# Performance work log

Hardware: AMD Instinct MI355X
Metric: run time of the kernel (lower is better)

Reference implementation:

```python
import jax, jax.numpy as jnp
import numpy as np

B, T, V, E, H = 256, 512, 30000, 256, 32


def _run_dir(x, mask, Wih, Whh, bih, bhh, reverse):
    # x: [B,T,D], mask: [B,T] bool. PyTorch GRU gate order: r, z, n.
    gi = jnp.einsum('btd,gd->btg', x, Wih) + bih  # precompute input gates [B,T,3H]
    h0 = jnp.zeros((x.shape[0], Whh.shape[1]), x.dtype)

    def step(h, inp):
        gi_t, m_t = inp
        gh = h @ Whh.T + bhh
        ir, iz, inn = jnp.split(gi_t, 3, axis=-1)
        hr, hz, hn = jnp.split(gh, 3, axis=-1)
        r = jax.nn.sigmoid(ir + hr)
        z = jax.nn.sigmoid(iz + hz)
        n = jnp.tanh(inn + r * hn)
        h_new = (1.0 - z) * n + z * h
        # packed-sequence semantics: freeze state at padded steps
        h = jnp.where(m_t[:, None], h_new, h)
        return h, h

    hT, ys = jax.lax.scan(step, h0, (jnp.swapaxes(gi, 0, 1), mask.T), reverse=reverse)
    return jnp.swapaxes(ys, 0, 1), hT  # outputs [B,T,H], final hidden [B,H]


def _bigru_layer(x, mask, pf, pb):
    of, hf = _run_dir(x, mask, *pf, reverse=False)
    ob, hb = _run_dir(x, mask, *pb, reverse=True)
    return jnp.concatenate([of, ob], axis=-1), hf, hb


def setup_inputs() -> dict:
    key = jax.random.key(0)
    ks = jax.random.split(key, 24)
    lengths = jax.random.randint(ks[0], (B,), 1, T + 1)
    mask = (jnp.arange(T)[None, :] < lengths[:, None]).astype(jnp.int32)
    ids = jax.random.randint(ks[1], (B, T), 1, V)
    ids = jnp.where(mask > 0, ids, 0)  # pad_id = 0 at padded positions
    embed = (jax.random.normal(ks[2], (V, E), jnp.float32) * 0.1).at[0].set(0.0)

    def gru_params(k, din):
        k1, k2, k3, k4 = jax.random.split(k, 4)
        s = 1.0 / np.sqrt(H)
        return (jax.random.uniform(k1, (3 * H, din), jnp.float32, -s, s),
                jax.random.uniform(k2, (3 * H, H), jnp.float32, -s, s),
                jax.random.uniform(k3, (3 * H,), jnp.float32, -s, s),
                jax.random.uniform(k4, (3 * H,), jnp.float32, -s, s))

    inp = {"input_ids": ids, "attention_mask": mask, "embed": embed}
    i = 3
    for layer, din in (("l0", E), ("l1", 2 * H)):
        for d in ("f", "b"):
            Wih, Whh, bih, bhh = gru_params(ks[i], din); i += 1
            inp[f"Wih_{layer}{d}"] = Wih
            inp[f"Whh_{layer}{d}"] = Whh
            inp[f"bih_{layer}{d}"] = bih
            inp[f"bhh_{layer}{d}"] = bhh
    s = 1.0 / np.sqrt(2 * H)
    inp["Wout"] = jax.random.uniform(ks[i], (6, 2 * H), jnp.float32, -s, s)
    inp["bout"] = jax.random.uniform(ks[i + 1], (6,), jnp.float32, -s, s)
    return inp


def reference(input_ids, attention_mask, embed,
              Wih_l0f, Whh_l0f, bih_l0f, bhh_l0f,
              Wih_l0b, Whh_l0b, bih_l0b, bhh_l0b,
              Wih_l1f, Whh_l1f, bih_l1f, bhh_l1f,
              Wih_l1b, Whh_l1b, bih_l1b, bhh_l1b,
              Wout, bout):
    mask = attention_mask > 0
    x = embed[input_ids]  # [B,T,E]
    x1, _, _ = _bigru_layer(x, mask,
                            (Wih_l0f, Whh_l0f, bih_l0f, bhh_l0f),
                            (Wih_l0b, Whh_l0b, bih_l0b, bhh_l0b))
    # no dropout: eval-mode forward
    _, hf, hb = _bigru_layer(x1, mask,
                             (Wih_l1f, Whh_l1f, bih_l1f, bhh_l1f),
                             (Wih_l1b, Whh_l1b, bih_l1b, bhh_l1b))
    top = jnp.concatenate([hf, hb], axis=-1)  # h_n[-2:] -> [B, 2H]
    return top @ Wout.T + bout  # [B, 6]
```

## Files before the change

### kernel.cpp

```cpp
#include <hip/hip_runtime.h>
#include <hip/hip_bf16.h>

#define B_ 256
#define T_ 512
#define V_ 30000
#define E_ 256
#define H_ 32

__device__ __forceinline__ float sigmoidf_fast(float x) {
    return 1.0f / (1.0f + __expf(-x));
}
__device__ __forceinline__ float tanhf_fast(float x) {
    return 1.0f - 2.0f / (1.0f + __expf(2.0f * x));
}
__device__ __forceinline__ float rl(float v, int lane) {
    return __int_as_float(__builtin_amdgcn_readlane(__float_as_int(v), lane));
}

#define GEMM_MT 64
#define GEMM_KC 32
#define GEMM_PA 68
#define GEMM_PB 196

__global__ __launch_bounds__(256) void gemm_gates(
    const float* __restrict__ A, int M, int K,
    const float* __restrict__ Wf, const float* __restrict__ Wb,
    const float* __restrict__ bihf, const float* __restrict__ bhhf,
    const float* __restrict__ bihb, const float* __restrict__ bhhb,
    float* __restrict__ Out)
{
    __shared__ float As[GEMM_KC][GEMM_PA];
    __shared__ float Bs[GEMM_KC][GEMM_PB];

    const int tid = threadIdx.x;
    const int mbase = blockIdx.x * GEMM_MT;
    const int mg = tid >> 5, ng = tid & 31;
    const int m_off = mg * 8, n_off = ng * 6;

    float acc[8][6];
    #pragma unroll
    for (int r = 0; r < 8; ++r)
        #pragma unroll
        for (int c = 0; c < 6; ++c) acc[r][c] = 0.f;

    for (int kc = 0; kc < K; kc += GEMM_KC) {
        #pragma unroll
        for (int i = 0; i < 2; ++i) {
            int fi = tid + 256 * i;
            int row = fi >> 3, cf = fi & 7;
            int m = mbase + row;
            float4 v = make_float4(0.f, 0.f, 0.f, 0.f);
            if (m < M) v = *(const float4*)&A[(size_t)m * K + kc + cf * 4];
            As[cf * 4 + 0][row] = v.x; As[cf * 4 + 1][row] = v.y;
            As[cf * 4 + 2][row] = v.z; As[cf * 4 + 3][row] = v.w;
        }
        #pragma unroll
        for (int i = 0; i < 6; ++i) {
            int fi = tid + 256 * i;
            int g = fi >> 3, cf = fi & 7;
            const float* Wsel = (g < 96) ? (Wf + (size_t)g * K)
                                         : (Wb + (size_t)(g - 96) * K);
            float4 v = *(const float4*)&Wsel[kc + cf * 4];
            Bs[cf * 4 + 0][g] = v.x; Bs[cf * 4 + 1][g] = v.y;
            Bs[cf * 4 + 2][g] = v.z; Bs[cf * 4 + 3][g] = v.w;
        }
        __syncthreads();
        #pragma unroll
        for (int k = 0; k < GEMM_KC; ++k) {
            float a[8], bb[6];
            *(float4*)&a[0] = *(const float4*)&As[k][m_off];
            *(float4*)&a[4] = *(const float4*)&As[k][m_off + 4];
            *(float2*)&bb[0] = *(const float2*)&Bs[k][n_off];
            *(float2*)&bb[2] = *(const float2*)&Bs[k][n_off + 2];
            *(float2*)&bb[4] = *(const float2*)&Bs[k][n_off + 4];
            #pragma unroll
            for (int r = 0; r < 8; ++r)
                #pragma unroll
                for (int c = 0; c < 6; ++c)
                    acc[r][c] = fmaf(a[r], bb[c], acc[r][c]);
        }
        __syncthreads();
    }

    float bias[6];
    #pragma unroll
    for (int c = 0; c < 6; ++c) {
        int g = n_off + c;
        int g96 = (g < 96) ? g : g - 96;
        const float* bih = (g < 96) ? bihf : bihb;
        const float* bhh = (g < 96) ? bhhf : bhhb;
        bias[c] = bih[g96] + ((g96 < 64) ? bhh[g96] : 0.f);
    }
    #pragma unroll
    for (int r = 0; r < 8; ++r) {
        int m = mbase + m_off + r;
        if (m < M) {
            float* op = &Out[(size_t)m * 192 + n_off];
            #pragma unroll
            for (int c = 0; c < 6; ++c) op[c] = acc[r][c] + bias[c];
        }
    }
}

template <int USE_IDS>
__global__ __launch_bounds__(64, 1) void gru_scan(
    const float* __restrict__ gi,
    const int* __restrict__ ids,
    const int* __restrict__ mask,
    const float* __restrict__ Whh_f, const float* __restrict__ Whh_b,
    const float* __restrict__ bhh_f, const float* __restrict__ bhh_b,
    float* __restrict__ out_seq,
    float* __restrict__ out_fin)
{
    const int l = threadIdx.x;
    const int j = l & 31;
    const bool lower = l < 32;
    const int dir = blockIdx.x & 1;
    const int b = blockIdx.x >> 1;
    const int bT = b * T_;

    const float* Whh = dir ? Whh_b : Whh_f;
    const float* bhh = dir ? bhh_b : bhh_f;

    const int rowA = lower ? j : (32 + j);
    float wA[32], wB[32];
    #pragma unroll
    for (int q = 0; q < 8; ++q) {
        float4 a = *(const float4*)&Whh[rowA * 32 + q * 4];
        wA[q * 4 + 0] = a.x; wA[q * 4 + 1] = a.y;
        wA[q * 4 + 2] = a.z; wA[q * 4 + 3] = a.w;
        float4 bq = *(const float4*)&Whh[(64 + j) * 32 + q * 4];
        wB[q * 4 + 0] = bq.x; wB[q * 4 + 1] = bq.y;
        wB[q * 4 + 2] = bq.z; wB[q * 4 + 3] = bq.w;
    }
    const float bn = bhh[64 + j];
    const int offA = dir * 96 + l;
    const int offB = dir * 96 + 64 + j;

    auto wbase = [&](int c) { return dir ? (bT + 508 - 4 * c) : (bT + 4 * c); };

    int4 ids0 = make_int4(0, 0, 0, 0);
    if (USE_IDS) ids0 = *(const int4*)&ids[wbase(0)];
    int4 mask_use = *(const int4*)&mask[wbase(0)];
    int4 mask_mid = *(const int4*)&mask[wbase(1)];
    int4 mask_in  = make_int4(0, 0, 0, 0);
    int4 ids_pf = make_int4(0, 0, 0, 0), ids_mid = ids_pf, ids_in = ids_pf;
    if (USE_IDS) {
        ids_pf  = *(const int4*)&ids[wbase(1)];
        ids_mid = *(const int4*)&ids[wbase(2)];
    }

    float gA[2][4], gB[2][4];
    #pragma unroll
    for (int u = 0; u < 4; ++u) {
        int row;
        if (USE_IDS) {
            const int* ip = (const int*)&ids0;
            row = dir ? ip[3 - u] : ip[u];
        } else {
            row = bT + (dir ? (511 - u) : u);
        }
        const float* gp = gi + (size_t)row * 192;
        gA[0][u] = gp[offA];
        gB[0][u] = gp[offB];
    }

    float h = 0.f;

    for (int c2 = 0; c2 < 64; ++c2) {
        #pragma unroll
        for (int p = 0; p < 2; ++p) {
            const int c = 2 * c2 + p;
            if (USE_IDS) {
                const int ci = (c + 3 < 128) ? (c + 3) : 127;
                ids_in = *(const int4*)&ids[wbase(ci)];
            }
            {
                const int cm = (c + 2 < 128) ? (c + 2) : 127;
                mask_in = *(const int4*)&mask[wbase(cm)];
            }
            const int cN = (c + 1 < 128) ? (c + 1) : 127;

            #pragma unroll
            for (int u = 0; u < 4; ++u) {
                int rowN;
                if (USE_IDS) {
                    const int* ip = (const int*)&ids_pf;
                    rowN = dir ? ip[3 - u] : ip[u];
                } else {
                    rowN = bT + (dir ? (511 - 4 * cN - u) : (4 * cN + u));
                }
                const float* gpN = gi + (size_t)rowN * 192;
                gA[p ^ 1][u] = gpN[offA];
                gB[p ^ 1][u] = gpN[offB];

                const int* mu = (const int*)&mask_use;
                const int m = dir ? mu[3 - u] : mu[u];

                float aA0 = 0.f, aA1 = 0.f, aA2 = 0.f, aA3 = 0.f;
                float aB0 = 0.f, aB1 = 0.f, aB2 = 0.f, aB3 = 0.f;
                #pragma unroll
                for (int k = 0; k < 32; k += 4) {
                    const float h0 = rl(h, k);
                    const float h1 = rl(h, k + 1);
                    const float h2 = rl(h, k + 2);
                    const float h3 = rl(h, k + 3);
                    aA0 = fmaf(wA[k],     h0, aA0);  aB0 = fmaf(wB[k],     h0, aB0);
                    aA1 = fmaf(wA[k + 1], h1, aA1);  aB1 = fmaf(wB[k + 1], h1, aB1);
                    aA2 = fmaf(wA[k + 2], h2, aA2);  aB2 = fmaf(wB[k + 2], h2, aB2);
                    aA3 = fmaf(wA[k + 3], h3, aA3);  aB3 = fmaf(wB[k + 3], h3, aB3);
                }
                const float dA = (aA0 + aA1) + (aA2 + aA3);
                const float dB = (aB0 + aB1) + (aB2 + aB3);

                const float s  = sigmoidf_fast(gA[p][u] + dA);
                const float hn = bn + dB;
                const float zz = __shfl_xor(s, 32, 64);
                const float n  = tanhf_fast(gB[p][u] + s * hn);
                const float hnew = n + zz * (h - n);
                h = m ? hnew : h;

                if (out_seq != nullptr) {
                    const int t = dir ? (511 - 4 * c - u) : (4 * c + u);
                    if (lower)
                        out_seq[(size_t)(bT + t) * 64 + dir * 32 + j] = h;
                }
            }
            mask_use = mask_mid; mask_mid = mask_in;
            if (USE_IDS) { ids_pf = ids_mid; ids_mid = ids_in; }
        }
    }

    if (out_fin != nullptr && lower)
        out_fin[b * 64 + dir * 32 + j] = h;
}

__global__ void head_kernel(const float* __restrict__ hfin,
                            const float* __restrict__ Wout,
                            const float* __restrict__ bout,
                            float* __restrict__ out)
{
    int idx = blockIdx.x * blockDim.x + threadIdx.x;
    if (idx >= B_ * 6) return;
    int b = idx / 6, o = idx % 6;
    float acc = bout[o];
    const float* hp = hfin + b * 64;
    const float* wp = Wout + o * 64;
    #pragma unroll
    for (int k = 0; k < 64; ++k) acc = fmaf(hp[k], wp[k], acc);
    out[idx] = acc;
}

extern "C" void kernel_launch(void* const* d_in, const int* in_sizes, int n_in,
                              void* d_out, int out_size, void* d_ws, size_t ws_size,
                              hipStream_t stream)
{
    const int*   ids   = (const int*)d_in[0];
    const int*   mask  = (const int*)d_in[1];
    const float* embed = (const float*)d_in[2];
    const float* Wih0f = (const float*)d_in[3];
    const float* Whh0f = (const float*)d_in[4];
    const float* bih0f = (const float*)d_in[5];
    const float* bhh0f = (const float*)d_in[6];
    const float* Wih0b = (const float*)d_in[7];
    const float* Whh0b = (const float*)d_in[8];
    const float* bih0b = (const float*)d_in[9];
    const float* bhh0b = (const float*)d_in[10];
    const float* Wih1f = (const float*)d_in[11];
    const float* Whh1f = (const float*)d_in[12];
    const float* bih1f = (const float*)d_in[13];
    const float* bhh1f = (const float*)d_in[14];
    const float* Wih1b = (const float*)d_in[15];
    const float* Whh1b = (const float*)d_in[16];
    const float* bih1b = (const float*)d_in[17];
    const float* bhh1b = (const float*)d_in[18];
    const float* Wout  = (const float*)d_in[19];
    const float* bout  = (const float*)d_in[20];

    float* ws   = (float*)d_ws;
    float* gbuf = ws;
    float* x1   = ws + (size_t)B_ * T_ * 192;
    float* hfin = x1 + (size_t)B_ * T_ * 64;

    gemm_gates<<<(V_ + GEMM_MT - 1) / GEMM_MT, 256, 0, stream>>>(
        embed, V_, E_, Wih0f, Wih0b, bih0f, bhh0f, bih0b, bhh0b, gbuf);

    gru_scan<1><<<2 * B_, 64, 0, stream>>>(
        gbuf, ids, mask, Whh0f, Whh0b, bhh0f, bhh0b, x1, nullptr);

    gemm_gates<<<(B_ * T_) / GEMM_MT, 256, 0, stream>>>(
        x1, B_ * T_, 64, Wih1f, Wih1b, bih1f, bhh1f, bih1b, bhh1b, gbuf);

    gru_scan<0><<<2 * B_, 64, 0, stream>>>(
        gbuf, nullptr, mask, Whh1f, Whh1b, bhh1f, bhh1b, nullptr, hfin);

    head_kernel<<<(B_ * 6 + 255) / 256, 256, 0, stream>>>(hfin, Wout, bout,
                                                          (float*)d_out);
}
```

Before: 577.4 us.

## Compute all three GRU gates per lane with packed FMA and drop cross-half shuffle

The recurrent step now has every lane compute all three gate dot products (r, z, n) for its hidden unit. It uses v_pk_fma_f32 with pairs of hidden values broadcast through SGPRs. This removes the lane split across the two half-waves and the __shfl_xor used to exchange z, shortening the serial dependency chain in each time step. The cost is more VGPRs for weights (96 floats per lane), the upper 32 lanes now doing redundant work, and inline asm that may constrain the compiler's scheduling.

```diff
diff --git a/kernel.cpp b/kernel.cpp
--- a/kernel.cpp
+++ b/kernel.cpp
@@ -1,5 +1,6 @@
 #include <hip/hip_runtime.h>
 #include <hip/hip_bf16.h>
+#include <stdint.h>
 
 #define B_ 256
 #define T_ 512
@@ -7,14 +8,19 @@
 #define E_ 256
 #define H_ 32
 
+typedef float v2f __attribute__((ext_vector_type(2)));
+
 __device__ __forceinline__ float sigmoidf_fast(float x) {
     return 1.0f / (1.0f + __expf(-x));
 }
 __device__ __forceinline__ float tanhf_fast(float x) {
     return 1.0f - 2.0f / (1.0f + __expf(2.0f * x));
 }
-__device__ __forceinline__ float rl(float v, int lane) {
-    return __int_as_float(__builtin_amdgcn_readlane(__float_as_int(v), lane));
+__device__ __forceinline__ uint32_t rlu(float v, int lane) {
+    return (uint32_t)__builtin_amdgcn_readlane(__float_as_int(v), lane);
+}
+__device__ __forceinline__ void pk_fma(v2f& acc, v2f w, uint64_t hh) {
+    asm("v_pk_fma_f32 %0, %1, %2, %0" : "+v"(acc) : "v"(w), "s"(hh));
 }
 
 #define GEMM_MT 64
@@ -122,20 +128,18 @@
     const float* Whh = dir ? Whh_b : Whh_f;
     const float* bhh = dir ? bhh_b : bhh_f;
 
-    const int rowA = lower ? j : (32 + j);
-    float wA[32], wB[32];
-    #pragma unroll
-    for (int q = 0; q < 8; ++q) {
-        float4 a = *(const float4*)&Whh[rowA * 32 + q * 4];
-        wA[q * 4 + 0] = a.x; wA[q * 4 + 1] = a.y;
-        wA[q * 4 + 2] = a.z; wA[q * 4 + 3] = a.w;
-        float4 bq = *(const float4*)&Whh[(64 + j) * 32 + q * 4];
-        wB[q * 4 + 0] = bq.x; wB[q * 4 + 1] = bq.y;
-        wB[q * 4 + 2] = bq.z; wB[q * 4 + 3] = bq.w;
+    v2f wR[16], wZ[16], wN[16];
+    #pragma unroll
+    for (int q = 0; q < 16; ++q) {
+        wR[q] = *(const v2f*)&Whh[j * 32 + 2 * q];
+        wZ[q] = *(const v2f*)&Whh[(32 + j) * 32 + 2 * q];
+        wN[q] = *(const v2f*)&Whh[(64 + j) * 32 + 2 * q];
     }
     const float bn = bhh[64 + j];
-    const int offA = dir * 96 + l;
-    const int offB = dir * 96 + 64 + j;
+
+    const int offR = dir * 96 + j;
+    const int offZ = dir * 96 + 32 + j;
+    const int offN = dir * 96 + 64 + j;
 
     auto wbase = [&](int c) { return dir ? (bT + 508 - 4 * c) : (bT + 4 * c); };
 
@@ -150,7 +154,7 @@
         ids_mid = *(const int4*)&ids[wbase(2)];
     }
 
-    float gA[2][4], gB[2][4];
+    float gR[2][4], gZ[2][4], gN[2][4];
     #pragma unroll
     for (int u = 0; u < 4; ++u) {
         int row;
@@ -161,8 +165,9 @@
             row = bT + (dir ? (511 - u) : u);
         }
         const float* gp = gi + (size_t)row * 192;
-        gA[0][u] = gp[offA];
-        gB[0][u] = gp[offB];
+        gR[0][u] = gp[offR];
+        gZ[0][u] = gp[offZ];
+        gN[0][u] = gp[offN];
     }
 
     float h = 0.f;
@@ -191,33 +196,28 @@
                     rowN = bT + (dir ? (511 - 4 * cN - u) : (4 * cN + u));
                 }
                 const float* gpN = gi + (size_t)rowN * 192;
-                gA[p ^ 1][u] = gpN[offA];
-                gB[p ^ 1][u] = gpN[offB];
+                gR[p ^ 1][u] = gpN[offR];
+                gZ[p ^ 1][u] = gpN[offZ];
+                gN[p ^ 1][u] = gpN[offN];
 
                 const int* mu = (const int*)&mask_use;
                 const int m = dir ? mu[3 - u] : mu[u];
 
-                float aA0 = 0.f, aA1 = 0.f, aA2 = 0.f, aA3 = 0.f;
-                float aB0 = 0.f, aB1 = 0.f, aB2 = 0.f, aB3 = 0.f;
+                v2f aR = {0.f, 0.f}, aZ = {0.f, 0.f}, aN = {0.f, 0.f};
                 #pragma unroll
-                for (int k = 0; k < 32; k += 4) {
-                    const float h0 = rl(h, k);
-                    const float h1 = rl(h, k + 1);
-                    const float h2 = rl(h, k + 2);
-                    const float h3 = rl(h, k + 3);
-                    aA0 = fmaf(wA[k],     h0, aA0);  aB0 = fmaf(wB[k],     h0, aB0);
-                    aA1 = fmaf(wA[k + 1], h1, aA1);  aB1 = fmaf(wB[k + 1], h1, aB1);
-                    aA2 = fmaf(wA[k + 2], h2, aA2);  aB2 = fmaf(wB[k + 2], h2, aB2);
-                    aA3 = fmaf(wA[k + 3], h3, aA3);  aB3 = fmaf(wB[k + 3], h3, aB3);
+                for (int k = 0; k < 16; ++k) {
+                    const uint32_t hlo = rlu(h, 2 * k);
+                    const uint32_t hhi = rlu(h, 2 * k + 1);
+                    const uint64_t hh = ((uint64_t)hhi << 32) | hlo;
+                    pk_fma(aR, wR[k], hh);
+                    pk_fma(aZ, wZ[k], hh);
+                    pk_fma(aN, wN[k], hh);
                 }
-                const float dA = (aA0 + aA1) + (aA2 + aA3);
-                const float dB = (aB0 + aB1) + (aB2 + aB3);
-
-                const float s  = sigmoidf_fast(gA[p][u] + dA);
-                const float hn = bn + dB;
-                const float zz = __shfl_xor(s, 32, 64);
-                const float n  = tanhf_fast(gB[p][u] + s * hn);
-                const float hnew = n + zz * (h - n);
+                const float r  = sigmoidf_fast(gR[p][u] + aR.x + aR.y);
+                const float z  = sigmoidf_fast(gZ[p][u] + aZ.x + aZ.y);
+                const float hn = bn + aN.x + aN.y;
+                const float n  = tanhf_fast(gN[p][u] + r * hn);
+                const float hnew = n + z * (h - n);
                 h = m ? hnew : h;
 
                 if (out_seq != nullptr) {
```

After: 563.3 us. 1.03x faster.
